# Kernel optimization log

Measured on AMD Instinct MI355X. Metric: run time of the kernel, lower is better.

The kernel has to match this reference:

```python
import jax, jax.numpy as jnp
import numpy as np

B, A, G = 256, 64, 978          # batch, n_atoms, num_gene
D_DRUG, D_CELL, D_DOSE = 128, 50, 128
CELL_IN, DOSE_IN = 978, 12
GLOBAL = D_DRUG + D_CELL + D_DOSE   # 306
EXP_IN = GLOBAL + 128               # 434
E, TOP_K = 4, 2


def setup_inputs() -> dict:
    key = jax.random.key(0)
    ks = jax.random.split(key, 24)
    w = lambda k, s: jax.random.normal(k, s, jnp.float32) * 0.05
    return {
        "drug_atom_embed": jax.random.normal(ks[0], (B, A, D_DRUG), jnp.float32),
        "input_cell_gex": jax.random.normal(ks[1], (B, CELL_IN), jnp.float32),
        "input_pert_idose": jax.random.normal(ks[2], (B, DOSE_IN), jnp.float32),
        # LinearEncoder: 978 -> 200 -> 100 -> 50 (ReLU after each)
        "cell_W1": w(ks[3], (CELL_IN, 200)), "cell_b1": jnp.zeros((200,), jnp.float32),
        "cell_W2": w(ks[4], (200, 100)),     "cell_b2": jnp.zeros((100,), jnp.float32),
        "cell_W3": w(ks[5], (100, D_CELL)),  "cell_b3": jnp.zeros((D_CELL,), jnp.float32),
        # DoseEncoder: 12 -> 64 -> 128 (ReLU after each; dropout off at eval)
        "dose_W1": w(ks[6], (DOSE_IN, 64)),  "dose_b1": jnp.zeros((64,), jnp.float32),
        "dose_W2": w(ks[7], (64, D_DOSE)),   "dose_b2": jnp.zeros((D_DOSE,), jnp.float32),
        # gene index embedding [num_gene, 128]
        "gene_emb": w(ks[8], (G, 128)),
        # GatingNetwork: 306 -> 128 -> 4
        "gate_W1": w(ks[9], (GLOBAL, 128)),  "gate_b1": jnp.zeros((128,), jnp.float32),
        "gate_W2": w(ks[10], (128, E)),      "gate_b2": jnp.zeros((E,), jnp.float32),
        # 4 ExpertNetworks stacked: 434 -> 128 -> 1
        "exp_W1": w(ks[11], (E, EXP_IN, 128)), "exp_b1": jnp.zeros((E, 128), jnp.float32),
        "exp_W2": w(ks[12], (E, 128, 1)),      "exp_b2": jnp.zeros((E, 1), jnp.float32),
    }


def reference(drug_atom_embed, input_cell_gex, input_pert_idose,
              cell_W1, cell_b1, cell_W2, cell_b2, cell_W3, cell_b3,
              dose_W1, dose_b1, dose_W2, dose_b2, gene_emb,
              gate_W1, gate_b1, gate_W2, gate_b2,
              exp_W1, exp_b1, exp_W2, exp_b2):
    relu = jax.nn.relu
    # drug: sum atom embeddings -> [B, 128]
    drug = drug_atom_embed.sum(axis=1)
    # cell encoder -> [B, 50]
    cell = relu(input_cell_gex @ cell_W1 + cell_b1)
    cell = relu(cell @ cell_W2 + cell_b2)
    cell = relu(cell @ cell_W3 + cell_b3)
    # dose encoder -> [B, 128]
    dose = relu(input_pert_idose @ dose_W1 + dose_b1)
    dose = relu(dose @ dose_W2 + dose_b2)
    # global features [B, 306]
    g = jnp.concatenate([drug, cell, dose], axis=1)
    # gating: top-k sparse gates [B, E]
    logits = relu(g @ gate_W1 + gate_b1) @ gate_W2 + gate_b2
    top_v, top_i = jax.lax.top_k(logits, TOP_K)
    top_g = jax.nn.softmax(top_v, axis=1)
    gates = jnp.zeros_like(logits).at[jnp.arange(logits.shape[0])[:, None], top_i].set(top_g)
    # gene-aware expert input [B, G, 434]
    expert_input = jnp.concatenate([
        jnp.broadcast_to(g[:, None, :], (g.shape[0], G, GLOBAL)),
        jnp.broadcast_to(gene_emb[None, :, :], (g.shape[0], G, 128)),
    ], axis=2)
    # all experts: [B, E, G, 128] -> [B, E, G]
    h = relu(jnp.einsum('bgi,eih->begh', expert_input, exp_W1) + exp_b1[None, :, None, :])
    o = jnp.einsum('begh,eho->beg', h, exp_W2) + exp_b2[None, :, :1]  # exp_b2[e,0] broadcast
    predictions = jnp.einsum('beg,be->bg', o, gates)
    return predictions, cell
```

## Files before the change

### kernel.cpp

```cpp
#include <hip/hip_runtime.h>

#define NB 256
#define NA 64
#define NG 978
#define CELL_IN 978
#define DOSE_IN 12
#define GLOBAL_F 306
#define EXP_IN 434
#define NE 4

#define WS_SEL 0
#define WS_U   (WS_SEL + NB*4)
#define WS_V   (WS_U + NB*256)

#define A_BLOCKS 256
#define AB_GRID  (NB + A_BLOCKS)

__device__ __forceinline__ float wave_reduce(float p) {
    #pragma unroll
    for (int off = 32; off > 0; off >>= 1) p += __shfl_down(p, off, 64);
    return p;
}

__device__ __forceinline__ float rfl(float x) {
    return __int_as_float(__builtin_amdgcn_readfirstlane(__float_as_int(x)));
}

__global__ __launch_bounds__(1024) void ab_kernel(
    const float* __restrict__ drug, const float* __restrict__ gex,
    const float* __restrict__ idose,
    const float* __restrict__ cW1, const float* __restrict__ cb1,
    const float* __restrict__ cW2, const float* __restrict__ cb2,
    const float* __restrict__ cW3, const float* __restrict__ cb3,
    const float* __restrict__ dW1, const float* __restrict__ db1,
    const float* __restrict__ dW2, const float* __restrict__ db2,
    const float* __restrict__ gW1, const float* __restrict__ gb1,
    const float* __restrict__ gW2, const float* __restrict__ gb2,
    const float* __restrict__ eW1, const float* __restrict__ eb1,
    const float* __restrict__ gene,
    float* __restrict__ ws, float* __restrict__ cell_out)
{
    __shared__ float s_gex[CELL_IN];
    __shared__ float s_g[GLOBAL_F];
    __shared__ float s_h1[200];
    __shared__ float s_h2[100];
    __shared__ float s_gh[128];
    __shared__ float s_d1[64];
    __shared__ int   s_isel[2];
    __shared__ float s_part[16 * 200];
    __shared__ float s_pu[32 * 128];
    __shared__ float s_gene[64 * 129];

    const int blk = blockIdx.x, tid = threadIdx.x;

    if (blk >= NB) {
        const int ablk = blk - NB;
        const int tile = ablk >> 4, e = (ablk >> 2) & 3, hq = ablk & 3;

        for (int i = tid; i < 64 * 128; i += 1024) {
            int gl = i >> 7, k = i & 127;
            int g = tile * 64 + gl;
            s_gene[gl * 129 + k] = (g < NG) ? gene[g * 128 + k] : 0.f;
        }
        __syncthreads();

        const int g_in  = tid & 63;
        const int slice = (tid >> 6) & 7;
        const int khalf = tid >> 9;
        const int h0 = hq * 32 + slice * 4;
        const float* wbase = eW1
            + ((size_t)e * EXP_IN + GLOBAL_F + khalf * 64) * 128 + h0;
        float4 acc = {0.f, 0.f, 0.f, 0.f};
        #pragma unroll 8
        for (int k = 0; k < 64; ++k) {
            float x = s_gene[g_in * 129 + khalf * 64 + k];
            float4 w = *(const float4*)(wbase + (size_t)k * 128);
            acc.x += x * w.x; acc.y += x * w.y; acc.z += x * w.z; acc.w += x * w.w;
        }
        *(float4*)&s_pu[(khalf * 512 + slice * 64 + g_in) * 4] = acc;
        __syncthreads();
        if (khalf == 0) {
            float4 a0 = *(const float4*)&s_pu[(slice * 64 + g_in) * 4];
            float4 a1 = *(const float4*)&s_pu[(512 + slice * 64 + g_in) * 4];
            float4 r = {a0.x + a1.x, a0.y + a1.y, a0.z + a1.z, a0.w + a1.w};
            const int q = hq * 8 + slice;
            float* vout = ws + WS_V
                + ((size_t)(tile * 4 + e)) * 8192 + q * 256 + g_in * 4;
            *(float4*)vout = r;
        }
        return;
    }

    const int b = blk;

    if (tid < CELL_IN) s_gex[tid] = gex[b * CELL_IN + tid];
    {
        int row = tid >> 7, d = tid & 127;
        const float* p = drug + ((size_t)b * NA) * 128 + d;
        float acc = 0.f;
        #pragma unroll
        for (int i = 0; i < 8; ++i) acc += p[(size_t)(i * 8 + row) * 128];
        s_pu[row * 128 + d] = acc;
    }
    __syncthreads();
    if (tid < 128) {
        float a = 0.f;
        #pragma unroll
        for (int r = 0; r < 8; ++r) a += s_pu[r * 128 + tid];
        s_g[tid] = a;
    } else if (tid < 192) {
        int j = tid - 128;
        float acc = db1[j];
        #pragma unroll
        for (int i = 0; i < DOSE_IN; ++i)
            acc += idose[b * DOSE_IN + i] * dW1[i * 64 + j];
        s_d1[j] = fmaxf(acc, 0.f);
    }
    __syncthreads();
    if (tid < 128) {
        float acc = db2[tid];
        #pragma unroll 8
        for (int i = 0; i < 64; ++i) acc += s_d1[i] * dW2[i * 128 + tid];
        s_g[178 + tid] = fmaxf(acc, 0.f);
    }
    __syncthreads();

    {
        int q = tid & 63, ks = tid >> 6;
        if (q < 50) {
            int i0 = ks * 62, i1 = min(i0 + 62, CELL_IN);
            float4 acc = {0.f, 0.f, 0.f, 0.f};
            #pragma unroll 4
            for (int i = i0; i < i1; ++i) {
                float4 w = *(const float4*)(cW1 + (size_t)i * 200 + 4 * q);
                float x = s_gex[i];
                acc.x += x * w.x; acc.y += x * w.y; acc.z += x * w.z; acc.w += x * w.w;
            }
            *(float4*)(&s_part[ks * 200 + 4 * q]) = acc;
        }
    }
    __syncthreads();
    if (tid < 200) {
        float a = cb1[tid];
        #pragma unroll
        for (int ks = 0; ks < 16; ++ks) a += s_part[ks * 200 + tid];
        s_h1[tid] = fmaxf(a, 0.f);
    }
    __syncthreads();

    {
        int q = tid & 31, ks = tid >> 5;
        if (q < 25 && ks < 16) {
            int i0 = ks * 13, i1 = min(i0 + 13, 200);
            float4 acc = {0.f, 0.f, 0.f, 0.f};
            #pragma unroll
            for (int i = i0; i < i1; ++i) {
                float4 w = *(const float4*)(cW2 + (size_t)i * 100 + 4 * q);
                float x = s_h1[i];
                acc.x += x * w.x; acc.y += x * w.y; acc.z += x * w.z; acc.w += x * w.w;
            }
            *(float4*)(&s_part[ks * 100 + 4 * q]) = acc;
        }
    }
    __syncthreads();
    if (tid < 100) {
        float a = cb2[tid];
        #pragma unroll
        for (int ks = 0; ks < 16; ++ks) a += s_part[ks * 100 + tid];
        s_h2[tid] = fmaxf(a, 0.f);
    }
    __syncthreads();

    {
        int j = tid & 63, ks = tid >> 6;
        if (j < 50 && ks < 8) {
            int i0 = ks * 13, i1 = min(i0 + 13, 100);
            float acc = 0.f;
            #pragma unroll
            for (int i = i0; i < i1; ++i) acc += s_h2[i] * cW3[i * 50 + j];
            s_part[ks * 64 + j] = acc;
        }
    }
    __syncthreads();
    if (tid < 50) {
        float a = cb3[tid];
        #pragma unroll
        for (int ks = 0; ks < 8; ++ks) a += s_part[ks * 64 + tid];
        float r = fmaxf(a, 0.f);
        s_g[128 + tid] = r;
        cell_out[b * 50 + tid] = r;
    }
    __syncthreads();

    {
        int q = tid & 31, ks = tid >> 5;
        if (ks < 16) {
            int i0 = ks * 20, i1 = min(i0 + 20, GLOBAL_F);
            float4 acc = {0.f, 0.f, 0.f, 0.f};
            #pragma unroll
            for (int i = i0; i < i1; ++i) {
                float4 w = *(const float4*)(gW1 + (size_t)i * 128 + 4 * q);
                float x = s_g[i];
                acc.x += x * w.x; acc.y += x * w.y; acc.z += x * w.z; acc.w += x * w.w;
            }
            *(float4*)(&s_part[ks * 128 + 4 * q]) = acc;
        }
    }
    __syncthreads();
    if (tid < 128) {
        float a = gb1[tid];
        #pragma unroll
        for (int ks = 0; ks < 16; ++ks) a += s_part[ks * 128 + tid];
        s_gh[tid] = fmaxf(a, 0.f);
    }
    __syncthreads();

    if (tid < 64) {
        float h0 = s_gh[tid], h1 = s_gh[tid + 64];
        float logit[NE];
        #pragma unroll
        for (int j = 0; j < NE; ++j) {
            float p = h0 * gW2[tid * NE + j] + h1 * gW2[(tid + 64) * NE + j];
            p = wave_reduce(p);
            logit[j] = p + gb2[j];
        }
        if (tid == 0) {
            int i1 = 0; float v1 = logit[0];
            #pragma unroll
            for (int i = 1; i < NE; ++i) if (logit[i] > v1) { v1 = logit[i]; i1 = i; }
            int i2 = -1; float v2 = -__builtin_inff();
            #pragma unroll
            for (int i = 0; i < NE; ++i) {
                if (i == i1) continue;
                if (logit[i] > v2) { v2 = logit[i]; i2 = i; }
            }
            float ex = __expf(v2 - v1);
            float inv = 1.f / (1.f + ex);
            s_isel[0] = i1; s_isel[1] = i2;
            ws[WS_SEL + b * 4 + 0] = (float)i1;
            ws[WS_SEL + b * 4 + 1] = (float)i2;
            ws[WS_SEL + b * 4 + 2] = inv;
            ws[WS_SEL + b * 4 + 3] = ex * inv;
        }
    }
    __syncthreads();

    {
        int es = tid >> 9, ks = (tid >> 5) & 15, h4 = tid & 31;
        int e = s_isel[es];
        int i0 = ks * 20, i1 = min(i0 + 20, GLOBAL_F);
        const float* wp = eW1 + (size_t)e * EXP_IN * 128 + 4 * h4;
        float4 acc = {0.f, 0.f, 0.f, 0.f};
        #pragma unroll
        for (int i = i0; i < i1; ++i) {
            float4 w = *(const float4*)(wp + (size_t)i * 128);
            float x = s_g[i];
            acc.x += x * w.x; acc.y += x * w.y; acc.z += x * w.z; acc.w += x * w.w;
        }
        *(float4*)(&s_pu[(es * 16 + ks) * 128 + 4 * h4]) = acc;
    }
    __syncthreads();
    if (tid < 256) {
        int es = tid >> 7, h = tid & 127;
        int e = s_isel[es];
        float a = eb1[e * 128 + h];
        #pragma unroll
        for (int ks = 0; ks < 16; ++ks) a += s_pu[(es * 16 + ks) * 128 + h];
        ws[WS_U + (size_t)b * 256 + es * 128 + h] = a;
    }
}

__global__ __launch_bounds__(256) void c_kernel(
    const float* __restrict__ eW2, const float* __restrict__ eb2,
    const float* __restrict__ ws, float* __restrict__ pred)
{
    const int b = blockIdx.x >> 2, quad = blockIdx.x & 3, tid = threadIdx.x;

    const float* sel = ws + WS_SEL + (size_t)b * 4;
    const int ea = __builtin_amdgcn_readfirstlane((int)sel[0]);
    const int eb = __builtin_amdgcn_readfirstlane((int)sel[1]);
    const float gA = rfl(sel[2]);
    const float gB = rfl(sel[3]);
    const float bA = eb2[ea], bB = eb2[eb];

    const float* pu = ws + WS_U + (size_t)b * 256;
    const float* wA = eW2 + ea * 128;
    const float* wB = eW2 + eb * 128;

    const int wv = tid >> 6, lane = tid & 63;
    const int tile = quad * 4 + wv;
    const float* vA = ws + WS_V + ((size_t)(tile * 4 + ea)) * 8192 + lane * 4;
    const float* vB = ws + WS_V + ((size_t)(tile * 4 + eb)) * 8192 + lane * 4;

    float dA = 0.f, dB = 0.f;
    #pragma unroll 8
    for (int q = 0; q < 32; ++q) {
        float4 va = *(const float4*)(vA + q * 256);
        float4 ua = *(const float4*)(pu + q * 4);
        float4 wa = *(const float4*)(wA + q * 4);
        dA += fmaxf(ua.x + va.x, 0.f) * wa.x + fmaxf(ua.y + va.y, 0.f) * wa.y
            + fmaxf(ua.z + va.z, 0.f) * wa.z + fmaxf(ua.w + va.w, 0.f) * wa.w;
        float4 vb = *(const float4*)(vB + q * 256);
        float4 ub = *(const float4*)(pu + 128 + q * 4);
        float4 wb = *(const float4*)(wB + q * 4);
        dB += fmaxf(ub.x + vb.x, 0.f) * wb.x + fmaxf(ub.y + vb.y, 0.f) * wb.y
            + fmaxf(ub.z + vb.z, 0.f) * wb.z + fmaxf(ub.w + vb.w, 0.f) * wb.w;
    }
    const int g = tile * 64 + lane;
    if (g < NG) pred[(size_t)b * NG + g] = gA * (dA + bA) + gB * (dB + bB);
}

extern "C" void kernel_launch(void* const* d_in, const int* in_sizes, int n_in,
                              void* d_out, int out_size, void* d_ws, size_t ws_size,
                              hipStream_t stream) {
    const float* drug  = (const float*)d_in[0];
    const float* gex   = (const float*)d_in[1];
    const float* idose = (const float*)d_in[2];
    const float* cW1 = (const float*)d_in[3];  const float* cb1 = (const float*)d_in[4];
    const float* cW2 = (const float*)d_in[5];  const float* cb2 = (const float*)d_in[6];
    const float* cW3 = (const float*)d_in[7];  const float* cb3 = (const float*)d_in[8];
    const float* dW1 = (const float*)d_in[9];  const float* db1 = (const float*)d_in[10];
    const float* dW2 = (const float*)d_in[11]; const float* db2 = (const float*)d_in[12];
    const float* gene = (const float*)d_in[13];
    const float* gW1 = (const float*)d_in[14]; const float* gb1 = (const float*)d_in[15];
    const float* gW2 = (const float*)d_in[16]; const float* gb2 = (const float*)d_in[17];
    const float* eW1 = (const float*)d_in[18]; const float* eb1 = (const float*)d_in[19];
    const float* eW2 = (const float*)d_in[20]; const float* eb2 = (const float*)d_in[21];

    float* ws   = (float*)d_ws;
    float* out  = (float*)d_out;
    float* pred = out;
    float* cell = out + NB * NG;

    ab_kernel<<<AB_GRID, 1024, 0, stream>>>(drug, gex, idose,
        cW1, cb1, cW2, cb2, cW3, cb3, dW1, db1, dW2, db2,
        gW1, gb1, gW2, gb2, eW1, eb1, gene, ws, cell);
    c_kernel<<<NB * 4, 256, 0, stream>>>(eW2, eb2, ws, pred);
}
```

Measured before the change: 153.5 us.

## Process four batch rows per block in encoder/gating stage to reuse weights

Each encoder/gating block now handles four batch rows instead of one. Activations are stored batch-interleaved in shared memory so each weight float4 loaded from global memory feeds four samples. Shared memory is merged into one aliased buffer. This cuts redundant weight reads (notably the 978x200 cell weights) by four and shrinks the B-block grid from 256 to 64. The cost is fewer blocks for parallelism and longer per-block serial chains.

```diff
diff --git a/kernel.cpp b/kernel.cpp
--- a/kernel.cpp
+++ b/kernel.cpp
@@ -9,12 +9,25 @@
 #define EXP_IN 434
 #define NE 4
 
+#define NBATCH 4
+#define B_BLOCKS (NB / NBATCH)
+#define A_BLOCKS 256
+#define AB_GRID  (B_BLOCKS + A_BLOCKS)
+
 #define WS_SEL 0
 #define WS_U   (WS_SEL + NB*4)
 #define WS_V   (WS_U + NB*256)
 
-#define A_BLOCKS 256
-#define AB_GRID  (NB + A_BLOCKS)
+#define SMEM_F 15296
+#define O_GEXT 0
+#define O_GT   3912
+#define O_H1T  5136
+#define O_H2T  5936
+#define O_D1   6336
+#define O_GH   6592
+#define O_PART 7104
+#define O_GENE 0
+#define O_PUA  8256
 
 __device__ __forceinline__ float wave_reduce(float p) {
     #pragma unroll
@@ -40,21 +53,15 @@
     const float* __restrict__ gene,
     float* __restrict__ ws, float* __restrict__ cell_out)
 {
-    __shared__ float s_gex[CELL_IN];
-    __shared__ float s_g[GLOBAL_F];
-    __shared__ float s_h1[200];
-    __shared__ float s_h2[100];
-    __shared__ float s_gh[128];
-    __shared__ float s_d1[64];
-    __shared__ int   s_isel[2];
-    __shared__ float s_part[16 * 200];
-    __shared__ float s_pu[32 * 128];
-    __shared__ float s_gene[64 * 129];
+    __shared__ float smem[SMEM_F];
+    __shared__ int   s_isel[NBATCH][2];
 
     const int blk = blockIdx.x, tid = threadIdx.x;
 
-    if (blk >= NB) {
-        const int ablk = blk - NB;
+    if (blk >= B_BLOCKS) {
+        float* s_gene = smem + O_GENE;
+        float* s_pu_a = smem + O_PUA;
+        const int ablk = blk - B_BLOCKS;
         const int tile = ablk >> 4, e = (ablk >> 2) & 3, hq = ablk & 3;
 
         for (int i = tid; i < 64 * 128; i += 1024) {
@@ -77,11 +84,11 @@
             float4 w = *(const float4*)(wbase + (size_t)k * 128);
             acc.x += x * w.x; acc.y += x * w.y; acc.z += x * w.z; acc.w += x * w.w;
         }
-        *(float4*)&s_pu[(khalf * 512 + slice * 64 + g_in) * 4] = acc;
+        *(float4*)&s_pu_a[(khalf * 512 + slice * 64 + g_in) * 4] = acc;
         __syncthreads();
         if (khalf == 0) {
-            float4 a0 = *(const float4*)&s_pu[(slice * 64 + g_in) * 4];
-            float4 a1 = *(const float4*)&s_pu[(512 + slice * 64 + g_in) * 4];
+            float4 a0 = *(const float4*)&s_pu_a[(slice * 64 + g_in) * 4];
+            float4 a1 = *(const float4*)&s_pu_a[(512 + slice * 64 + g_in) * 4];
             float4 r = {a0.x + a1.x, a0.y + a1.y, a0.z + a1.z, a0.w + a1.w};
             const int q = hq * 8 + slice;
             float* vout = ws + WS_V
@@ -91,140 +98,176 @@
         return;
     }
 
-    const int b = blk;
-
-    if (tid < CELL_IN) s_gex[tid] = gex[b * CELL_IN + tid];
-    {
-        int row = tid >> 7, d = tid & 127;
-        const float* p = drug + ((size_t)b * NA) * 128 + d;
+    const int b0 = blk * NBATCH;
+    float* s_gexT = smem + O_GEXT;
+    float* s_gT   = smem + O_GT;
+    float* s_h1T  = smem + O_H1T;
+    float* s_h2T  = smem + O_H2T;
+    float* s_d1   = smem + O_D1;
+    float* s_gh   = smem + O_GH;
+    float* s_part = smem + O_PART;
+
+    #pragma unroll
+    for (int bb = 0; bb < NBATCH; ++bb)
+        for (int k = tid; k < CELL_IN; k += 1024)
+            s_gexT[k * 4 + bb] = gex[(size_t)(b0 + bb) * CELL_IN + k];
+    {
+        int bl = tid >> 8, ah = (tid >> 7) & 1, d = tid & 127;
+        const float* p = drug + ((size_t)(b0 + bl) * NA + ah * 32) * 128 + d;
         float acc = 0.f;
         #pragma unroll
-        for (int i = 0; i < 8; ++i) acc += p[(size_t)(i * 8 + row) * 128];
-        s_pu[row * 128 + d] = acc;
-    }
-    __syncthreads();
-    if (tid < 128) {
-        float a = 0.f;
-        #pragma unroll
-        for (int r = 0; r < 8; ++r) a += s_pu[r * 128 + tid];
-        s_g[tid] = a;
-    } else if (tid < 192) {
-        int j = tid - 128;
+        for (int i = 0; i < 32; ++i) acc += p[(size_t)i * 128];
+        s_part[bl * 256 + ah * 128 + d] = acc;
+    }
+    __syncthreads();
+    if (tid < 512) {
+        int bl = tid >> 7, d = tid & 127;
+        s_gT[d * 4 + bl] = s_part[bl * 256 + d] + s_part[bl * 256 + 128 + d];
+    } else if (tid < 768) {
+        int idx = tid - 512, bl = idx >> 6, j = idx & 63;
         float acc = db1[j];
         #pragma unroll
         for (int i = 0; i < DOSE_IN; ++i)
-            acc += idose[b * DOSE_IN + i] * dW1[i * 64 + j];
-        s_d1[j] = fmaxf(acc, 0.f);
-    }
-    __syncthreads();
-    if (tid < 128) {
-        float acc = db2[tid];
+            acc += idose[(b0 + bl) * DOSE_IN + i] * dW1[i * 64 + j];
+        s_d1[bl * 64 + j] = fmaxf(acc, 0.f);
+    }
+    __syncthreads();
+    if (tid < 512) {
+        int bl = tid >> 7, j = tid & 127;
+        float acc = db2[j];
         #pragma unroll 8
-        for (int i = 0; i < 64; ++i) acc += s_d1[i] * dW2[i * 128 + tid];
-        s_g[178 + tid] = fmaxf(acc, 0.f);
-    }
-    __syncthreads();
-
-    {
-        int q = tid & 63, ks = tid >> 6;
+        for (int i = 0; i < 64; ++i) acc += s_d1[bl * 64 + i] * dW2[i * 128 + j];
+        s_gT[(178 + j) * 4 + bl] = fmaxf(acc, 0.f);
+    }
+    __syncthreads();
+
+    if (tid < 512) {
+        int ks = tid >> 6, q = tid & 63;
         if (q < 50) {
-            int i0 = ks * 62, i1 = min(i0 + 62, CELL_IN);
-            float4 acc = {0.f, 0.f, 0.f, 0.f};
+            int k0 = ks * 123, k1 = min(k0 + 123, CELL_IN);
+            float4 a0 = {0,0,0,0}, a1 = {0,0,0,0}, a2 = {0,0,0,0}, a3 = {0,0,0,0};
             #pragma unroll 4
-            for (int i = i0; i < i1; ++i) {
-                float4 w = *(const float4*)(cW1 + (size_t)i * 200 + 4 * q);
-                float x = s_gex[i];
-                acc.x += x * w.x; acc.y += x * w.y; acc.z += x * w.z; acc.w += x * w.w;
+            for (int k = k0; k < k1; ++k) {
+                float4 x = *(const float4*)&s_gexT[k * 4];
+                float4 w = *(const float4*)(cW1 + (size_t)k * 200 + 4 * q);
+                a0.x += x.x * w.x; a0.y += x.x * w.y; a0.z += x.x * w.z; a0.w += x.x * w.w;
+                a1.x += x.y * w.x; a1.y += x.y * w.y; a1.z += x.y * w.z; a1.w += x.y * w.w;
+                a2.x += x.z * w.x; a2.y += x.z * w.y; a2.z += x.z * w.z; a2.w += x.z * w.w;
+                a3.x += x.w * w.x; a3.y += x.w * w.y; a3.z += x.w * w.z; a3.w += x.w * w.w;
             }
-            *(float4*)(&s_part[ks * 200 + 4 * q]) = acc;
-        }
-    }
-    __syncthreads();
-    if (tid < 200) {
-        float a = cb1[tid];
-        #pragma unroll
-        for (int ks = 0; ks < 16; ++ks) a += s_part[ks * 200 + tid];
-        s_h1[tid] = fmaxf(a, 0.f);
-    }
-    __syncthreads();
-
-    {
-        int q = tid & 31, ks = tid >> 5;
-        if (q < 25 && ks < 16) {
-            int i0 = ks * 13, i1 = min(i0 + 13, 200);
-            float4 acc = {0.f, 0.f, 0.f, 0.f};
-            #pragma unroll
-            for (int i = i0; i < i1; ++i) {
-                float4 w = *(const float4*)(cW2 + (size_t)i * 100 + 4 * q);
-                float x = s_h1[i];
-                acc.x += x * w.x; acc.y += x * w.y; acc.z += x * w.z; acc.w += x * w.w;
+            *(float4*)&s_part[(ks * 4 + 0) * 200 + 4 * q] = a0;
+            *(float4*)&s_part[(ks * 4 + 1) * 200 + 4 * q] = a1;
+            *(float4*)&s_part[(ks * 4 + 2) * 200 + 4 * q] = a2;
+            *(float4*)&s_part[(ks * 4 + 3) * 200 + 4 * q] = a3;
+        }
+    }
+    __syncthreads();
+    {
+        int b = tid >> 8, j = tid & 255;
+        if (j < 200) {
+            float a = cb1[j];
+            #pragma unroll
+            for (int ks = 0; ks < 8; ++ks) a += s_part[(ks * 4 + b) * 200 + j];
+            s_h1T[j * 4 + b] = fmaxf(a, 0.f);
+        }
+    }
+    __syncthreads();
+
+    if (tid < 512) {
+        int ks = tid >> 5, q = tid & 31;
+        if (q < 25) {
+            int k0 = ks * 13, k1 = min(k0 + 13, 200);
+            float4 a0 = {0,0,0,0}, a1 = {0,0,0,0}, a2 = {0,0,0,0}, a3 = {0,0,0,0};
+            #pragma unroll
+            for (int k = k0; k < k1; ++k) {
+                float4 x = *(const float4*)&s_h1T[k * 4];
+                float4 w = *(const float4*)(cW2 + (size_t)k * 100 + 4 * q);
+                a0.x += x.x * w.x; a0.y += x.x * w.y; a0.z += x.x * w.z; a0.w += x.x * w.w;
+                a1.x += x.y * w.x; a1.y += x.y * w.y; a1.z += x.y * w.z; a1.w += x.y * w.w;
+                a2.x += x.z * w.x; a2.y += x.z * w.y; a2.z += x.z * w.z; a2.w += x.z * w.w;
+                a3.x += x.w * w.x; a3.y += x.w * w.y; a3.z += x.w * w.z; a3.w += x.w * w.w;
             }
-            *(float4*)(&s_part[ks * 100 + 4 * q]) = acc;
-        }
-    }
-    __syncthreads();
-    if (tid < 100) {
-        float a = cb2[tid];
-        #pragma unroll
-        for (int ks = 0; ks < 16; ++ks) a += s_part[ks * 100 + tid];
-        s_h2[tid] = fmaxf(a, 0.f);
-    }
-    __syncthreads();
-
-    {
-        int j = tid & 63, ks = tid >> 6;
-        if (j < 50 && ks < 8) {
-            int i0 = ks * 13, i1 = min(i0 + 13, 100);
+            *(float4*)&s_part[(ks * 4 + 0) * 100 + 4 * q] = a0;
+            *(float4*)&s_part[(ks * 4 + 1) * 100 + 4 * q] = a1;
+            *(float4*)&s_part[(ks * 4 + 2) * 100 + 4 * q] = a2;
+            *(float4*)&s_part[(ks * 4 + 3) * 100 + 4 * q] = a3;
+        }
+    }
+    __syncthreads();
+    if (tid < 512) {
+        int b = tid >> 7, j = tid & 127;
+        if (j < 100) {
+            float a = cb2[j];
+            #pragma unroll
+            for (int ks = 0; ks < 16; ++ks) a += s_part[(ks * 4 + b) * 100 + j];
+            s_h2T[j * 4 + b] = fmaxf(a, 0.f);
+        }
+    }
+    __syncthreads();
+
+    {
+        int ks = tid >> 8, b = (tid >> 6) & 3, j = tid & 63;
+        if (j < 50) {
+            int k0 = ks * 25, k1 = k0 + 25;
             float acc = 0.f;
             #pragma unroll
-            for (int i = i0; i < i1; ++i) acc += s_h2[i] * cW3[i * 50 + j];
-            s_part[ks * 64 + j] = acc;
-        }
-    }
-    __syncthreads();
-    if (tid < 50) {
-        float a = cb3[tid];
-        #pragma unroll
-        for (int ks = 0; ks < 8; ++ks) a += s_part[ks * 64 + tid];
-        float r = fmaxf(a, 0.f);
-        s_g[128 + tid] = r;
-        cell_out[b * 50 + tid] = r;
-    }
-    __syncthreads();
-
-    {
-        int q = tid & 31, ks = tid >> 5;
-        if (ks < 16) {
-            int i0 = ks * 20, i1 = min(i0 + 20, GLOBAL_F);
-            float4 acc = {0.f, 0.f, 0.f, 0.f};
-            #pragma unroll
-            for (int i = i0; i < i1; ++i) {
-                float4 w = *(const float4*)(gW1 + (size_t)i * 128 + 4 * q);
-                float x = s_g[i];
-                acc.x += x * w.x; acc.y += x * w.y; acc.z += x * w.z; acc.w += x * w.w;
-            }
-            *(float4*)(&s_part[ks * 128 + 4 * q]) = acc;
-        }
-    }
-    __syncthreads();
-    if (tid < 128) {
-        float a = gb1[tid];
-        #pragma unroll
-        for (int ks = 0; ks < 16; ++ks) a += s_part[ks * 128 + tid];
-        s_gh[tid] = fmaxf(a, 0.f);
-    }
-    __syncthreads();
-
-    if (tid < 64) {
-        float h0 = s_gh[tid], h1 = s_gh[tid + 64];
+            for (int k = k0; k < k1; ++k) acc += s_h2T[k * 4 + b] * cW3[k * 50 + j];
+            s_part[(ks * 4 + b) * 64 + j] = acc;
+        }
+    }
+    __syncthreads();
+    if (tid < 256) {
+        int b = tid >> 6, j = tid & 63;
+        if (j < 50) {
+            float a = cb3[j];
+            #pragma unroll
+            for (int ks = 0; ks < 4; ++ks) a += s_part[(ks * 4 + b) * 64 + j];
+            float r = fmaxf(a, 0.f);
+            s_gT[(128 + j) * 4 + b] = r;
+            cell_out[(b0 + b) * 50 + j] = r;
+        }
+    }
+    __syncthreads();
+
+    if (tid < 512) {
+        int ks = tid >> 5, q = tid & 31;
+        int k0 = ks * 20, k1 = min(k0 + 20, GLOBAL_F);
+        float4 a0 = {0,0,0,0}, a1 = {0,0,0,0}, a2 = {0,0,0,0}, a3 = {0,0,0,0};
+        #pragma unroll
+        for (int k = k0; k < k1; ++k) {
+            float4 x = *(const float4*)&s_gT[k * 4];
+            float4 w = *(const float4*)(gW1 + (size_t)k * 128 + 4 * q);
+            a0.x += x.x * w.x; a0.y += x.x * w.y; a0.z += x.x * w.z; a0.w += x.x * w.w;
+            a1.x += x.y * w.x; a1.y += x.y * w.y; a1.z += x.y * w.z; a1.w += x.y * w.w;
+            a2.x += x.z * w.x; a2.y += x.z * w.y; a2.z += x.z * w.z; a2.w += x.z * w.w;
+            a3.x += x.w * w.x; a3.y += x.w * w.y; a3.z += x.w * w.z; a3.w += x.w * w.w;
+        }
+        *(float4*)&s_part[(ks * 4 + 0) * 128 + 4 * q] = a0;
+        *(float4*)&s_part[(ks * 4 + 1) * 128 + 4 * q] = a1;
+        *(float4*)&s_part[(ks * 4 + 2) * 128 + 4 * q] = a2;
+        *(float4*)&s_part[(ks * 4 + 3) * 128 + 4 * q] = a3;
+    }
+    __syncthreads();
+    if (tid < 512) {
+        int b = tid >> 7, h = tid & 127;
+        float a = gb1[h];
+        #pragma unroll
+        for (int ks = 0; ks < 16; ++ks) a += s_part[(ks * 4 + b) * 128 + h];
+        s_gh[b * 128 + h] = fmaxf(a, 0.f);
+    }
+    __syncthreads();
+
+    if (tid < 256) {
+        int bl = tid >> 6, lane = tid & 63;
+        float h0 = s_gh[bl * 128 + lane], h1 = s_gh[bl * 128 + 64 + lane];
         float logit[NE];
         #pragma unroll
         for (int j = 0; j < NE; ++j) {
-            float p = h0 * gW2[tid * NE + j] + h1 * gW2[(tid + 64) * NE + j];
+            float p = h0 * gW2[lane * NE + j] + h1 * gW2[(lane + 64) * NE + j];
             p = wave_reduce(p);
             logit[j] = p + gb2[j];
         }
-        if (tid == 0) {
+        if (lane == 0) {
             int i1 = 0; float v1 = logit[0];
             #pragma unroll
             for (int i = 1; i < NE; ++i) if (logit[i] > v1) { v1 = logit[i]; i1 = i; }
@@ -236,37 +279,39 @@
             }
             float ex = __expf(v2 - v1);
             float inv = 1.f / (1.f + ex);
-            s_isel[0] = i1; s_isel[1] = i2;
-            ws[WS_SEL + b * 4 + 0] = (float)i1;
-            ws[WS_SEL + b * 4 + 1] = (float)i2;
-            ws[WS_SEL + b * 4 + 2] = inv;
-            ws[WS_SEL + b * 4 + 3] = ex * inv;
-        }
-    }
-    __syncthreads();
-
-    {
-        int es = tid >> 9, ks = (tid >> 5) & 15, h4 = tid & 31;
-        int e = s_isel[es];
-        int i0 = ks * 20, i1 = min(i0 + 20, GLOBAL_F);
-        const float* wp = eW1 + (size_t)e * EXP_IN * 128 + 4 * h4;
-        float4 acc = {0.f, 0.f, 0.f, 0.f};
-        #pragma unroll
-        for (int i = i0; i < i1; ++i) {
-            float4 w = *(const float4*)(wp + (size_t)i * 128);
-            float x = s_g[i];
+            s_isel[bl][0] = i1; s_isel[bl][1] = i2;
+            int bg = b0 + bl;
+            ws[WS_SEL + bg * 4 + 0] = (float)i1;
+            ws[WS_SEL + bg * 4 + 1] = (float)i2;
+            ws[WS_SEL + bg * 4 + 2] = inv;
+            ws[WS_SEL + bg * 4 + 3] = ex * inv;
+        }
+    }
+    __syncthreads();
+
+    {
+        int bl = tid >> 8, es = (tid >> 7) & 1, ks = (tid >> 5) & 3, q = tid & 31;
+        int e = s_isel[bl][es];
+        int k0 = ks * 77, k1 = min(k0 + 77, GLOBAL_F);
+        const float* wp = eW1 + (size_t)e * EXP_IN * 128 + 4 * q;
+        float4 acc = {0,0,0,0};
+        #pragma unroll 4
+        for (int k = k0; k < k1; ++k) {
+            float x = s_gT[k * 4 + bl];
+            float4 w = *(const float4*)(wp + (size_t)k * 128);
             acc.x += x * w.x; acc.y += x * w.y; acc.z += x * w.z; acc.w += x * w.w;
         }
-        *(float4*)(&s_pu[(es * 16 + ks) * 128 + 4 * h4]) = acc;
-    }
-    __syncthreads();
-    if (tid < 256) {
-        int es = tid >> 7, h = tid & 127;
-        int e = s_isel[es];
+        *(float4*)&s_part[((bl * 2 + es) * 4 + ks) * 128 + 4 * q] = acc;
+    }
+    __syncthreads();
+    {
+        int bl = tid >> 8, es = (tid >> 7) & 1, h = tid & 127;
+        int e = s_isel[bl][es];
         float a = eb1[e * 128 + h];
         #pragma unroll
-        for (int ks = 0; ks < 16; ++ks) a += s_pu[(es * 16 + ks) * 128 + h];
-        ws[WS_U + (size_t)b * 256 + es * 128 + h] = a;
+        for (int ks = 0; ks < 4; ++ks)
+            a += s_part[((bl * 2 + es) * 4 + ks) * 128 + h];
+        ws[WS_U + (size_t)(b0 + bl) * 256 + es * 128 + h] = a;
     }
 }
 
```

New measurement: 157.4 us. 1.03x slower.

## Split per-sample MLP chain into batched multi-kernel stages reusing weights across 8 samples

Applied to the files above, without the earlier changes.

Replaces the one-block-per-sample encoder/gating/expert-U pipeline with three kernels that process 8 samples per block, using a transposed feature layout in workspace. Each weight element loaded from global memory is now reused across 8 batch rows, cutting weight traffic, and the cell-layer-1 matmul is split across output slices for more parallelism. The expert U projection is now computed for all 4 experts instead of only the selected two, so it no longer waits for gating. The cost is two extra kernel launches, extra global round-trips through workspace, and redundant expert-U work.

```diff
diff --git a/kernel.cpp b/kernel.cpp
--- a/kernel.cpp
+++ b/kernel.cpp
@@ -11,10 +11,15 @@
 
 #define WS_SEL 0
 #define WS_U   (WS_SEL + NB*4)
-#define WS_V   (WS_U + NB*256)
-
-#define A_BLOCKS 256
-#define AB_GRID  (NB + A_BLOCKS)
+#define WS_V   (WS_U + NB*4*128)
+#define WS_GT  (WS_V + 524288)
+#define WS_H1T (WS_GT + GLOBAL_F*NB)
+
+#define K1_A0   0
+#define K1_C10  256
+#define K1_DR0  384
+#define K1_DO0  640
+#define K1_GRID 672
 
 __device__ __forceinline__ float wave_reduce(float p) {
     #pragma unroll
@@ -26,36 +31,22 @@
     return __int_as_float(__builtin_amdgcn_readfirstlane(__float_as_int(x)));
 }
 
-__global__ __launch_bounds__(1024) void ab_kernel(
+__global__ __launch_bounds__(1024) void k1_kernel(
     const float* __restrict__ drug, const float* __restrict__ gex,
     const float* __restrict__ idose,
     const float* __restrict__ cW1, const float* __restrict__ cb1,
-    const float* __restrict__ cW2, const float* __restrict__ cb2,
-    const float* __restrict__ cW3, const float* __restrict__ cb3,
     const float* __restrict__ dW1, const float* __restrict__ db1,
     const float* __restrict__ dW2, const float* __restrict__ db2,
-    const float* __restrict__ gW1, const float* __restrict__ gb1,
-    const float* __restrict__ gW2, const float* __restrict__ gb2,
-    const float* __restrict__ eW1, const float* __restrict__ eb1,
-    const float* __restrict__ gene,
-    float* __restrict__ ws, float* __restrict__ cell_out)
+    const float* __restrict__ eW1, const float* __restrict__ gene,
+    float* __restrict__ ws)
 {
-    __shared__ float s_gex[CELL_IN];
-    __shared__ float s_g[GLOBAL_F];
-    __shared__ float s_h1[200];
-    __shared__ float s_h2[100];
-    __shared__ float s_gh[128];
-    __shared__ float s_d1[64];
-    __shared__ int   s_isel[2];
-    __shared__ float s_part[16 * 200];
-    __shared__ float s_pu[32 * 128];
-    __shared__ float s_gene[64 * 129];
-
+    __shared__ float smem[14224];
     const int blk = blockIdx.x, tid = threadIdx.x;
 
-    if (blk >= NB) {
-        const int ablk = blk - NB;
-        const int tile = ablk >> 4, e = (ablk >> 2) & 3, hq = ablk & 3;
+    if (blk < K1_C10) {
+        float* s_gene = smem;
+        float* s_pu   = smem + 8256;
+        const int tile = blk >> 4, e = (blk >> 2) & 3, hq = blk & 3;
 
         for (int i = tid; i < 64 * 128; i += 1024) {
             int gl = i >> 7, k = i & 127;
@@ -91,140 +82,247 @@
         return;
     }
 
-    const int b = blk;
-
-    if (tid < CELL_IN) s_gex[tid] = gex[b * CELL_IN + tid];
-    {
-        int row = tid >> 7, d = tid & 127;
+    if (blk < K1_DR0) {
+        const int idx = blk - K1_C10;
+        const int mg = idx >> 2, ns = idx & 3;
+        const int b0 = mg * 8;
+        float* s_x = smem;
+        float* s_p = smem + 7824;
+
+        for (int i = tid; i < CELL_IN * 8; i += 1024) {
+            int k = i >> 3, bb = i & 7;
+            s_x[i] = gex[(size_t)(b0 + bb) * CELL_IN + k];
+        }
+        __syncthreads();
+
+        const int ks = tid >> 6, lane = tid & 63;
+        if (lane < 50) {
+            const int n = ns * 50 + lane;
+            int k0 = ks * 62, k1 = min(k0 + 62, CELL_IN);
+            float a0=0,a1=0,a2=0,a3=0,a4=0,a5=0,a6=0,a7=0;
+            #pragma unroll 4
+            for (int k = k0; k < k1; ++k) {
+                float w = cW1[(size_t)k * 200 + n];
+                float4 xa = *(const float4*)&s_x[k * 8];
+                float4 xb = *(const float4*)&s_x[k * 8 + 4];
+                a0 += xa.x * w; a1 += xa.y * w; a2 += xa.z * w; a3 += xa.w * w;
+                a4 += xb.x * w; a5 += xb.y * w; a6 += xb.z * w; a7 += xb.w * w;
+            }
+            float* pp = &s_p[(ks * 50 + lane) * 8];
+            pp[0]=a0; pp[1]=a1; pp[2]=a2; pp[3]=a3;
+            pp[4]=a4; pp[5]=a5; pp[6]=a6; pp[7]=a7;
+        }
+        __syncthreads();
+        if (tid < 400) {
+            int n50 = tid >> 3, bb = tid & 7;
+            int n = ns * 50 + n50;
+            float a = cb1[n];
+            #pragma unroll
+            for (int k = 0; k < 16; ++k) a += s_p[(k * 50 + n50) * 8 + bb];
+            ws[WS_H1T + (size_t)n * NB + b0 + bb] = fmaxf(a, 0.f);
+        }
+        return;
+    }
+
+    if (blk < K1_DO0) {
+        const int b = blk - K1_DR0;
+        float* s_red = smem;
+        const int r = tid >> 7, d = tid & 127;
         const float* p = drug + ((size_t)b * NA) * 128 + d;
         float acc = 0.f;
         #pragma unroll
-        for (int i = 0; i < 8; ++i) acc += p[(size_t)(i * 8 + row) * 128];
-        s_pu[row * 128 + d] = acc;
-    }
-    __syncthreads();
-    if (tid < 128) {
-        float a = 0.f;
+        for (int i = 0; i < 8; ++i) acc += p[(size_t)(i * 8 + r) * 128];
+        s_red[r * 128 + d] = acc;
+        __syncthreads();
+        if (tid < 128) {
+            float a = 0.f;
+            #pragma unroll
+            for (int rr = 0; rr < 8; ++rr) a += s_red[rr * 128 + tid];
+            ws[WS_GT + (size_t)tid * NB + b] = a;
+        }
+        return;
+    }
+
+    {
+        const int mg = blk - K1_DO0;
+        const int b0 = mg * 8;
+        float* s_d1 = smem;
+        const int bb = tid >> 7, j = tid & 127;
+        if (j < 64) {
+            float acc = db1[j];
+            #pragma unroll
+            for (int i = 0; i < DOSE_IN; ++i)
+                acc += idose[(b0 + bb) * DOSE_IN + i] * dW1[i * 64 + j];
+            s_d1[bb * 64 + j] = fmaxf(acc, 0.f);
+        }
+        __syncthreads();
+        float acc = db2[j];
+        #pragma unroll 8
+        for (int i = 0; i < 64; ++i) acc += s_d1[bb * 64 + i] * dW2[i * 128 + j];
+        ws[WS_GT + (size_t)(178 + j) * NB + b0 + bb] = fmaxf(acc, 0.f);
+    }
+}
+
+__global__ __launch_bounds__(1024) void k2_kernel(
+    const float* __restrict__ cW2, const float* __restrict__ cb2,
+    const float* __restrict__ cW3, const float* __restrict__ cb3,
+    float* __restrict__ ws, float* __restrict__ cell_out)
+{
+    __shared__ float s_x1[200 * 8];
+    __shared__ float s_p[8 * 100 * 8];
+    __shared__ float s_x2[100 * 8];
+    const int mg = blockIdx.x, tid = threadIdx.x;
+    const int b0 = mg * 8;
+
+    for (int i = tid; i < 200 * 8; i += 1024) {
+        int k = i >> 3, bb = i & 7;
+        s_x1[i] = ws[WS_H1T + (size_t)k * NB + b0 + bb];
+    }
+    __syncthreads();
+
+    {
+        const int ks = tid >> 7, j = tid & 127;
+        if (j < 100) {
+            int k0 = ks * 25, k1 = k0 + 25;
+            float a0=0,a1=0,a2=0,a3=0,a4=0,a5=0,a6=0,a7=0;
+            #pragma unroll 5
+            for (int k = k0; k < k1; ++k) {
+                float w = cW2[(size_t)k * 100 + j];
+                float4 xa = *(const float4*)&s_x1[k * 8];
+                float4 xb = *(const float4*)&s_x1[k * 8 + 4];
+                a0 += xa.x * w; a1 += xa.y * w; a2 += xa.z * w; a3 += xa.w * w;
+                a4 += xb.x * w; a5 += xb.y * w; a6 += xb.z * w; a7 += xb.w * w;
+            }
+            float* pp = &s_p[(ks * 100 + j) * 8];
+            pp[0]=a0; pp[1]=a1; pp[2]=a2; pp[3]=a3;
+            pp[4]=a4; pp[5]=a5; pp[6]=a6; pp[7]=a7;
+        }
+    }
+    __syncthreads();
+    if (tid < 800) {
+        int j = tid >> 3, bb = tid & 7;
+        float a = cb2[j];
         #pragma unroll
-        for (int r = 0; r < 8; ++r) a += s_pu[r * 128 + tid];
-        s_g[tid] = a;
-    } else if (tid < 192) {
-        int j = tid - 128;
-        float acc = db1[j];
+        for (int k = 0; k < 8; ++k) a += s_p[(k * 100 + j) * 8 + bb];
+        s_x2[j * 8 + bb] = fmaxf(a, 0.f);
+    }
+    __syncthreads();
+
+    {
+        const int ks = tid >> 7, j = tid & 127;
+        if (j < 50) {
+            int k0 = ks * 13, k1 = min(k0 + 13, 100);
+            float a0=0,a1=0,a2=0,a3=0,a4=0,a5=0,a6=0,a7=0;
+            #pragma unroll
+            for (int k = k0; k < k1; ++k) {
+                float w = cW3[(size_t)k * 50 + j];
+                float4 xa = *(const float4*)&s_x2[k * 8];
+                float4 xb = *(const float4*)&s_x2[k * 8 + 4];
+                a0 += xa.x * w; a1 += xa.y * w; a2 += xa.z * w; a3 += xa.w * w;
+                a4 += xb.x * w; a5 += xb.y * w; a6 += xb.z * w; a7 += xb.w * w;
+            }
+            float* pp = &s_p[(ks * 50 + j) * 8];
+            pp[0]=a0; pp[1]=a1; pp[2]=a2; pp[3]=a3;
+            pp[4]=a4; pp[5]=a5; pp[6]=a6; pp[7]=a7;
+        }
+    }
+    __syncthreads();
+    if (tid < 400) {
+        int j = tid >> 3, bb = tid & 7;
+        float a = cb3[j];
         #pragma unroll
-        for (int i = 0; i < DOSE_IN; ++i)
-            acc += idose[b * DOSE_IN + i] * dW1[i * 64 + j];
-        s_d1[j] = fmaxf(acc, 0.f);
-    }
-    __syncthreads();
-    if (tid < 128) {
-        float acc = db2[tid];
-        #pragma unroll 8
-        for (int i = 0; i < 64; ++i) acc += s_d1[i] * dW2[i * 128 + tid];
-        s_g[178 + tid] = fmaxf(acc, 0.f);
-    }
-    __syncthreads();
+        for (int k = 0; k < 8; ++k) a += s_p[(k * 50 + j) * 8 + bb];
+        float r = fmaxf(a, 0.f);
+        ws[WS_GT + (size_t)(128 + j) * NB + b0 + bb] = r;
+        cell_out[(b0 + bb) * 50 + j] = r;
+    }
+}
+
+__global__ __launch_bounds__(1024) void k3_kernel(
+    const float* __restrict__ gW1, const float* __restrict__ gb1,
+    const float* __restrict__ gW2, const float* __restrict__ gb2,
+    const float* __restrict__ eW1, const float* __restrict__ eb1,
+    float* __restrict__ ws)
+{
+    __shared__ float s_g[GLOBAL_F * 8];
+    __shared__ float s_p[8 * 128 * 8];
+    __shared__ float s_gh[128 * 8];
+    const int blk = blockIdx.x, tid = threadIdx.x;
+    const bool is_u = blk < 128;
+    const int mg = is_u ? (blk >> 2) : (blk - 128);
+    const int b0 = mg * 8;
+
+    for (int i = tid; i < GLOBAL_F * 8; i += 1024) {
+        int k = i >> 3, bb = i & 7;
+        s_g[i] = ws[WS_GT + (size_t)k * NB + b0 + bb];
+    }
+    __syncthreads();
+
+    if (is_u) {
+        const int e = blk & 3;
+        {
+            const int ks = tid >> 7, h = tid & 127;
+            int k0 = ks * 39, k1 = min(k0 + 39, GLOBAL_F);
+            float a0=0,a1=0,a2=0,a3=0,a4=0,a5=0,a6=0,a7=0;
+            #pragma unroll 4
+            for (int k = k0; k < k1; ++k) {
+                float w = eW1[((size_t)e * EXP_IN + k) * 128 + h];
+                float4 xa = *(const float4*)&s_g[k * 8];
+                float4 xb = *(const float4*)&s_g[k * 8 + 4];
+                a0 += xa.x * w; a1 += xa.y * w; a2 += xa.z * w; a3 += xa.w * w;
+                a4 += xb.x * w; a5 += xb.y * w; a6 += xb.z * w; a7 += xb.w * w;
+            }
+            float* pp = &s_p[(ks * 128 + h) * 8];
+            pp[0]=a0; pp[1]=a1; pp[2]=a2; pp[3]=a3;
+            pp[4]=a4; pp[5]=a5; pp[6]=a6; pp[7]=a7;
+        }
+        __syncthreads();
+        {
+            int h = tid >> 3, bb = tid & 7;
+            float a = eb1[e * 128 + h];
+            #pragma unroll
+            for (int k = 0; k < 8; ++k) a += s_p[(k * 128 + h) * 8 + bb];
+            ws[WS_U + ((size_t)(b0 + bb) * 4 + e) * 128 + h] = a;
+        }
+        return;
+    }
 
     {
-        int q = tid & 63, ks = tid >> 6;
-        if (q < 50) {
-            int i0 = ks * 62, i1 = min(i0 + 62, CELL_IN);
-            float4 acc = {0.f, 0.f, 0.f, 0.f};
-            #pragma unroll 4
-            for (int i = i0; i < i1; ++i) {
-                float4 w = *(const float4*)(cW1 + (size_t)i * 200 + 4 * q);
-                float x = s_gex[i];
-                acc.x += x * w.x; acc.y += x * w.y; acc.z += x * w.z; acc.w += x * w.w;
-            }
-            *(float4*)(&s_part[ks * 200 + 4 * q]) = acc;
-        }
-    }
-    __syncthreads();
-    if (tid < 200) {
-        float a = cb1[tid];
+        const int ks = tid >> 7, h = tid & 127;
+        int k0 = ks * 39, k1 = min(k0 + 39, GLOBAL_F);
+        float a0=0,a1=0,a2=0,a3=0,a4=0,a5=0,a6=0,a7=0;
+        #pragma unroll 4
+        for (int k = k0; k < k1; ++k) {
+            float w = gW1[(size_t)k * 128 + h];
+            float4 xa = *(const float4*)&s_g[k * 8];
+            float4 xb = *(const float4*)&s_g[k * 8 + 4];
+            a0 += xa.x * w; a1 += xa.y * w; a2 += xa.z * w; a3 += xa.w * w;
+            a4 += xb.x * w; a5 += xb.y * w; a6 += xb.z * w; a7 += xb.w * w;
+        }
+        float* pp = &s_p[(ks * 128 + h) * 8];
+        pp[0]=a0; pp[1]=a1; pp[2]=a2; pp[3]=a3;
+        pp[4]=a4; pp[5]=a5; pp[6]=a6; pp[7]=a7;
+    }
+    __syncthreads();
+    {
+        int h = tid >> 3, bb = tid & 7;
+        float a = gb1[h];
         #pragma unroll
-        for (int ks = 0; ks < 16; ++ks) a += s_part[ks * 200 + tid];
-        s_h1[tid] = fmaxf(a, 0.f);
-    }
-    __syncthreads();
-
-    {
-        int q = tid & 31, ks = tid >> 5;
-        if (q < 25 && ks < 16) {
-            int i0 = ks * 13, i1 = min(i0 + 13, 200);
-            float4 acc = {0.f, 0.f, 0.f, 0.f};
-            #pragma unroll
-            for (int i = i0; i < i1; ++i) {
-                float4 w = *(const float4*)(cW2 + (size_t)i * 100 + 4 * q);
-                float x = s_h1[i];
-                acc.x += x * w.x; acc.y += x * w.y; acc.z += x * w.z; acc.w += x * w.w;
-            }
-            *(float4*)(&s_part[ks * 100 + 4 * q]) = acc;
-        }
-    }
-    __syncthreads();
-    if (tid < 100) {
-        float a = cb2[tid];
-        #pragma unroll
-        for (int ks = 0; ks < 16; ++ks) a += s_part[ks * 100 + tid];
-        s_h2[tid] = fmaxf(a, 0.f);
-    }
-    __syncthreads();
-
-    {
-        int j = tid & 63, ks = tid >> 6;
-        if (j < 50 && ks < 8) {
-            int i0 = ks * 13, i1 = min(i0 + 13, 100);
-            float acc = 0.f;
-            #pragma unroll
-            for (int i = i0; i < i1; ++i) acc += s_h2[i] * cW3[i * 50 + j];
-            s_part[ks * 64 + j] = acc;
-        }
-    }
-    __syncthreads();
-    if (tid < 50) {
-        float a = cb3[tid];
-        #pragma unroll
-        for (int ks = 0; ks < 8; ++ks) a += s_part[ks * 64 + tid];
-        float r = fmaxf(a, 0.f);
-        s_g[128 + tid] = r;
-        cell_out[b * 50 + tid] = r;
-    }
-    __syncthreads();
-
-    {
-        int q = tid & 31, ks = tid >> 5;
-        if (ks < 16) {
-            int i0 = ks * 20, i1 = min(i0 + 20, GLOBAL_F);
-            float4 acc = {0.f, 0.f, 0.f, 0.f};
-            #pragma unroll
-            for (int i = i0; i < i1; ++i) {
-                float4 w = *(const float4*)(gW1 + (size_t)i * 128 + 4 * q);
-                float x = s_g[i];
-                acc.x += x * w.x; acc.y += x * w.y; acc.z += x * w.z; acc.w += x * w.w;
-            }
-            *(float4*)(&s_part[ks * 128 + 4 * q]) = acc;
-        }
-    }
-    __syncthreads();
-    if (tid < 128) {
-        float a = gb1[tid];
-        #pragma unroll
-        for (int ks = 0; ks < 16; ++ks) a += s_part[ks * 128 + tid];
-        s_gh[tid] = fmaxf(a, 0.f);
-    }
-    __syncthreads();
-
-    if (tid < 64) {
-        float h0 = s_gh[tid], h1 = s_gh[tid + 64];
+        for (int k = 0; k < 8; ++k) a += s_p[(k * 128 + h) * 8 + bb];
+        s_gh[h * 8 + bb] = fmaxf(a, 0.f);
+    }
+    __syncthreads();
+    if (tid < 512) {
+        int bb = tid >> 6, lane = tid & 63;
+        float h0 = s_gh[lane * 8 + bb], h1 = s_gh[(lane + 64) * 8 + bb];
         float logit[NE];
         #pragma unroll
         for (int j = 0; j < NE; ++j) {
-            float p = h0 * gW2[tid * NE + j] + h1 * gW2[(tid + 64) * NE + j];
+            float p = h0 * gW2[lane * NE + j] + h1 * gW2[(lane + 64) * NE + j];
             p = wave_reduce(p);
             logit[j] = p + gb2[j];
         }
-        if (tid == 0) {
+        if (lane == 0) {
             int i1 = 0; float v1 = logit[0];
             #pragma unroll
             for (int i = 1; i < NE; ++i) if (logit[i] > v1) { v1 = logit[i]; i1 = i; }
@@ -236,37 +334,12 @@
             }
             float ex = __expf(v2 - v1);
             float inv = 1.f / (1.f + ex);
-            s_isel[0] = i1; s_isel[1] = i2;
-            ws[WS_SEL + b * 4 + 0] = (float)i1;
-            ws[WS_SEL + b * 4 + 1] = (float)i2;
-            ws[WS_SEL + b * 4 + 2] = inv;
-            ws[WS_SEL + b * 4 + 3] = ex * inv;
-        }
-    }
-    __syncthreads();
-
-    {
-        int es = tid >> 9, ks = (tid >> 5) & 15, h4 = tid & 31;
-        int e = s_isel[es];
-        int i0 = ks * 20, i1 = min(i0 + 20, GLOBAL_F);
-        const float* wp = eW1 + (size_t)e * EXP_IN * 128 + 4 * h4;
-        float4 acc = {0.f, 0.f, 0.f, 0.f};
-        #pragma unroll
-        for (int i = i0; i < i1; ++i) {
-            float4 w = *(const float4*)(wp + (size_t)i * 128);
-            float x = s_g[i];
-            acc.x += x * w.x; acc.y += x * w.y; acc.z += x * w.z; acc.w += x * w.w;
-        }
-        *(float4*)(&s_pu[(es * 16 + ks) * 128 + 4 * h4]) = acc;
-    }
-    __syncthreads();
-    if (tid < 256) {
-        int es = tid >> 7, h = tid & 127;
-        int e = s_isel[es];
-        float a = eb1[e * 128 + h];
-        #pragma unroll
-        for (int ks = 0; ks < 16; ++ks) a += s_pu[(es * 16 + ks) * 128 + h];
-        ws[WS_U + (size_t)b * 256 + es * 128 + h] = a;
+            int bg = b0 + bb;
+            ws[WS_SEL + bg * 4 + 0] = (float)i1;
+            ws[WS_SEL + bg * 4 + 1] = (float)i2;
+            ws[WS_SEL + bg * 4 + 2] = inv;
+            ws[WS_SEL + bg * 4 + 3] = ex * inv;
+        }
     }
 }
 
@@ -283,7 +356,8 @@
     const float gB = rfl(sel[3]);
     const float bA = eb2[ea], bB = eb2[eb];
 
-    const float* pu = ws + WS_U + (size_t)b * 256;
+    const float* uA = ws + WS_U + ((size_t)b * 4 + ea) * 128;
+    const float* uB = ws + WS_U + ((size_t)b * 4 + eb) * 128;
     const float* wA = eW2 + ea * 128;
     const float* wB = eW2 + eb * 128;
 
@@ -296,12 +370,12 @@
     #pragma unroll 8
     for (int q = 0; q < 32; ++q) {
         float4 va = *(const float4*)(vA + q * 256);
-        float4 ua = *(const float4*)(pu + q * 4);
+        float4 ua = *(const float4*)(uA + q * 4);
         float4 wa = *(const float4*)(wA + q * 4);
         dA += fmaxf(ua.x + va.x, 0.f) * wa.x + fmaxf(ua.y + va.y, 0.f) * wa.y
             + fmaxf(ua.z + va.z, 0.f) * wa.z + fmaxf(ua.w + va.w, 0.f) * wa.w;
         float4 vb = *(const float4*)(vB + q * 256);
-        float4 ub = *(const float4*)(pu + 128 + q * 4);
+        float4 ub = *(const float4*)(uB + q * 4);
         float4 wb = *(const float4*)(wB + q * 4);
         dB += fmaxf(ub.x + vb.x, 0.f) * wb.x + fmaxf(ub.y + vb.y, 0.f) * wb.y
             + fmaxf(ub.z + vb.z, 0.f) * wb.z + fmaxf(ub.w + vb.w, 0.f) * wb.w;
@@ -332,8 +406,9 @@
     float* pred = out;
     float* cell = out + NB * NG;
 
-    ab_kernel<<<AB_GRID, 1024, 0, stream>>>(drug, gex, idose,
-        cW1, cb1, cW2, cb2, cW3, cb3, dW1, db1, dW2, db2,
-        gW1, gb1, gW2, gb2, eW1, eb1, gene, ws, cell);
+    k1_kernel<<<K1_GRID, 1024, 0, stream>>>(drug, gex, idose,
+        cW1, cb1, dW1, db1, dW2, db2, eW1, gene, ws);
+    k2_kernel<<<32, 1024, 0, stream>>>(cW2, cb2, cW3, cb3, ws, cell);
+    k3_kernel<<<160, 1024, 0, stream>>>(gW1, gb1, gW2, gb2, eW1, eb1, ws);
     c_kernel<<<NB * 4, 256, 0, stream>>>(eW2, eb2, ws, pred);
 }
```

Result: no change. 151.4 us (-1.3%).
